# Kernel tuning notes

Measured on AMD Instinct MI355X. Metric: run time of the kernel, lower is better.

Reference implementation:

```python
import jax, jax.numpy as jnp
import numpy as np

M, K, D = 4, 2048, 32
N, C, H, W = 8, M * D, 64, 64


def setup_inputs() -> dict:
    key = jax.random.key(0)
    k1, k2 = jax.random.split(key)
    latent = jax.random.normal(k1, (N, C, H, W), dtype=jnp.float32)
    codebook = jax.random.normal(k2, (M, K, D), dtype=jnp.float32)
    return {"latent": latent, "codebook": codebook}


def reference(latent, codebook):
    n, c, h, w = latent.shape
    m, k, d = codebook.shape
    # [n,C,h,w] -> [n,h,w,m,d]
    q = jnp.transpose(latent, (0, 2, 3, 1)).reshape(n, h, w, m, d)
    q2 = jnp.sum(q * q, axis=-1, keepdims=True)          # [n,h,w,m,1]
    c2 = jnp.sum(codebook * codebook, axis=-1)           # [m,k]
    inter = jnp.einsum('nhwmd,mkd->nhwmk', q, codebook)  # [n,h,w,m,k]
    distance = -(q2 + c2 - 2.0 * inter)
    return jnp.argmax(distance, axis=-1)                 # [n,h,w,m] int
```

## Files before the change

### kernel.cpp

```cpp
#include <hip/hip_runtime.h>

#define M_ 4
#define K_ 2048
#define D_ 32
#define HW_ 4096
#define NHW_ 32768

#define EPS 0.01f

#define CH_OFF 0
#define CL_OFF (M_*K_*D_*2)
#define HN_OFF (CL_OFF*2)
#define K1_OFF (HN_OFF + M_*K_*4)
#define B2_OFF (K1_OFF + M_*NHW_*4)
#define CNT_OFF (B2_OFF + M_*NHW_*4)
#define LIST_OFF (CNT_OFF + 16)

typedef __attribute__((ext_vector_type(8))) short bf16x8;
typedef __attribute__((ext_vector_type(4))) float f32x4;

__device__ __forceinline__ short bf16_rte(float x, float* back) {
    unsigned u = __float_as_uint(x);
    unsigned r = (u + 0x7FFFu + ((u >> 16) & 1u)) >> 16;
    *back = __uint_as_float(r << 16);
    return (short)(r & 0xFFFFu);
}

__global__ __launch_bounds__(256) void prep_kernel(const float* __restrict__ cb,
                                                   unsigned char* __restrict__ ws) {
    if (blockIdx.x == 0 && threadIdx.x == 0) *(int*)(ws + CNT_OFF) = 0;
    int t = blockIdx.x * 256 + threadIdx.x;
    const float* src = cb + (size_t)t * D_;
    short* dh = (short*)(ws + CH_OFF) + (size_t)t * D_;
    short* dl = (short*)(ws + CL_OFF) + (size_t)t * D_;
    float* hn = (float*)(ws + HN_OFF);
    bf16x8 vh[4], vl[4];
    float c2 = 0.f;
    #pragma unroll
    for (int d = 0; d < D_; ++d) {
        float x = src[d];
        float hf, lf;
        short hb = bf16_rte(x, &hf);
        short lb = bf16_rte(x - hf, &lf);
        vh[d >> 3][d & 7] = hb;
        vl[d >> 3][d & 7] = lb;
        c2 = fmaf(x, x, c2);
    }
    #pragma unroll
    for (int i = 0; i < 4; ++i) {
        *(bf16x8*)(dh + i * 8) = vh[i];
        *(bf16x8*)(dl + i * 8) = vl[i];
    }
    hn[t] = -0.5f * c2;
}

__device__ __forceinline__ float score_fp32(const float* __restrict__ q,
                                            const float4* __restrict__ c) {
    float d0 = 0, d1 = 0, d2 = 0, d3 = 0, e0 = 0, e1 = 0, e2 = 0, e3 = 0;
    #pragma unroll
    for (int v = 0; v < 8; ++v) {
        float4 cv = c[v];
        d0 = fmaf(q[v * 4 + 0], cv.x, d0);
        d1 = fmaf(q[v * 4 + 1], cv.y, d1);
        d2 = fmaf(q[v * 4 + 2], cv.z, d2);
        d3 = fmaf(q[v * 4 + 3], cv.w, d3);
        e0 = fmaf(cv.x, cv.x, e0);
        e1 = fmaf(cv.y, cv.y, e1);
        e2 = fmaf(cv.z, cv.z, e2);
        e3 = fmaf(cv.w, cv.w, e3);
    }
    return ((d0 + d1) + (d2 + d3)) - 0.5f * ((e0 + e1) + (e2 + e3));
}

__global__ __launch_bounds__(512, 4) void score_kernel(
        const float* __restrict__ latent,
        const unsigned char* __restrict__ cws,
        int* __restrict__ k1w, float* __restrict__ b2w) {
    __shared__ float s_b1[2][M_][64];
    __shared__ int   s_k1[2][M_][64];
    __shared__ float s_b2[2][M_][64];

    const int tid  = threadIdx.x;
    const int wave = tid >> 6;
    const int L    = tid & 63;
    const int m    = wave & 3;
    const int kh   = wave >> 2;
    const int col  = L & 15;
    const int krow = L >> 4;
    const int posbase = blockIdx.x * 64;
    const int n   = posbase >> 12;
    const int hwb = posbase & (HW_ - 1);

    bf16x8 qh[4], ql[4];
    const float* lp = latent + ((size_t)n * (M_ * D_) + m * D_) * HW_ + hwb;
    #pragma unroll
    for (int g = 0; g < 4; ++g)
        #pragma unroll
        for (int j = 0; j < 8; ++j) {
            float x = lp[(size_t)(krow * 8 + j) * HW_ + g * 16 + col];
            float hf, lf;
            qh[g][j] = bf16_rte(x, &hf);
            ql[g][j] = bf16_rte(x - hf, &lf);
        }

    const short* ah = (const short*)(cws + CH_OFF)
                      + ((size_t)m * K_ + kh * 1024 + col) * D_ + krow * 8;
    const short* al = (const short*)(cws + CL_OFF)
                      + ((size_t)m * K_ + kh * 1024 + col) * D_ + krow * 8;
    const float* hn = (const float*)(cws + HN_OFF) + m * K_ + kh * 1024 + krow * 4;

    float b1[4], b2[4];
    int   k1[4];
    #pragma unroll
    for (int g = 0; g < 4; ++g) { b1[g] = b2[g] = -3.402823466e+38f; k1[g] = 0; }

    const int kbase = kh * 1024 + krow * 4;

    #pragma unroll 2
    for (int t = 0; t < 64; ++t) {
        bf16x8 ch = *(const bf16x8*)(ah + (size_t)t * (16 * D_));
        bf16x8 cl = *(const bf16x8*)(al + (size_t)t * (16 * D_));
        f32x4  c0 = *(const f32x4*)(hn + t * 16);
        const int kt = kbase + t * 16;
        #pragma unroll
        for (int g = 0; g < 4; ++g) {
            f32x4 a = __builtin_amdgcn_mfma_f32_16x16x32_bf16(cl, qh[g], c0, 0, 0, 0);
            a = __builtin_amdgcn_mfma_f32_16x16x32_bf16(ch, ql[g], a, 0, 0, 0);
            a = __builtin_amdgcn_mfma_f32_16x16x32_bf16(ch, qh[g], a, 0, 0, 0);
            #pragma unroll
            for (int r = 0; r < 4; ++r) {
                float s = a[r];
                b2[g] = __builtin_amdgcn_fmed3f(b1[g], b2[g], s);
                bool gt = s > b1[g];
                k1[g] = gt ? (kt + r) : k1[g];
                b1[g] = gt ? s : b1[g];
            }
        }
    }

    #pragma unroll
    for (int g = 0; g < 4; ++g) {
        #pragma unroll
        for (int off = 16; off <= 32; off <<= 1) {
            float ob1 = __shfl_xor(b1[g], off);
            int   ok1 = __shfl_xor(k1[g], off);
            float ob2 = __shfl_xor(b2[g], off);
            float mn  = fminf(b1[g], ob1);
            b2[g] = fmaxf(mn, fmaxf(b2[g], ob2));
            bool awin = (b1[g] > ob1) || (b1[g] == ob1 && k1[g] < ok1);
            b1[g] = awin ? b1[g] : ob1;
            k1[g] = awin ? k1[g] : ok1;
        }
    }
    if (L < 16) {
        #pragma unroll
        for (int g = 0; g < 4; ++g) {
            s_b1[kh][m][g * 16 + L] = b1[g];
            s_k1[kh][m][g * 16 + L] = k1[g];
            s_b2[kh][m][g * 16 + L] = b2[g];
        }
    }
    __syncthreads();

    if (tid < 256) {
        const int mm = tid >> 6;
        const int pl = tid & 63;
        float A1 = s_b1[0][mm][pl]; int I1 = s_k1[0][mm][pl]; float A2 = s_b2[0][mm][pl];
        float B1 = s_b1[1][mm][pl]; int J1 = s_k1[1][mm][pl]; float B2 = s_b2[1][mm][pl];
        float b2m = fmaxf(fminf(A1, B1), fmaxf(A2, B2));
        bool awin = (A1 > B1) || (A1 == B1 && I1 < J1);
        int K1 = awin ? I1 : J1;
        k1w[mm * NHW_ + posbase + pl] = K1;
        b2w[mm * NHW_ + posbase + pl] = b2m;
    }
}

__global__ __launch_bounds__(256) void confirm_kernel(
        const float* __restrict__ latent,
        const float* __restrict__ codebook,
        const int* __restrict__ k1w, const float* __restrict__ b2w,
        int* __restrict__ cnt, int* __restrict__ list,
        int* __restrict__ out) {
    const int t   = blockIdx.x * 256 + threadIdx.x;
    const int L   = threadIdx.x & 63;
    const int mm  = t >> 15;
    const int pos = t & (NHW_ - 1);
    const int n   = pos >> 12;
    const int hw  = pos & (HW_ - 1);

    int   K1  = k1w[t];
    float b2m = b2w[t];

    const float* lq = latent + ((size_t)n * (M_ * D_) + mm * D_) * HW_ + hw;
    float q[D_];
    #pragma unroll
    for (int d = 0; d < D_; ++d) q[d] = lq[(size_t)d * HW_];
    float sx = score_fp32(q, (const float4*)(codebook + ((size_t)mm * K_ + K1) * D_));
    bool conf = (sx > b2m + EPS);

    out[(size_t)pos * M_ + mm] = K1;

    unsigned long long mask = __ballot(!conf);
    if (mask) {
        int leader = __ffsll(mask) - 1;
        int base = 0;
        if (L == leader) base = atomicAdd(cnt, (int)__popcll(mask));
        base = __shfl(base, leader);
        if (!conf) {
            unsigned long long below = mask & ((1ull << L) - 1ull);
            list[base + (int)__popcll(below)] = t;
        }
    }
}

__global__ __launch_bounds__(256) void fallback_kernel(
        const float* __restrict__ latent,
        const float* __restrict__ codebook,
        const int* __restrict__ cnt, const int* __restrict__ list,
        int* __restrict__ out) {
    __shared__ float s_bs[4];
    __shared__ int   s_bk[4];
    const int tid  = threadIdx.x;
    const int wave = tid >> 6;
    const int L    = tid & 63;
    const int ncnt = *cnt;

    for (int e = blockIdx.x; e < ncnt; e += gridDim.x) {
        int t   = list[e];
        int mm  = t >> 15;
        int pos = t & (NHW_ - 1);
        int n   = pos >> 12;
        int hw  = pos & (HW_ - 1);
        const float* lq = latent + ((size_t)n * (M_ * D_) + mm * D_) * HW_ + hw;
        float q[D_];
        #pragma unroll
        for (int d = 0; d < D_; ++d) q[d] = lq[(size_t)d * HW_];

        float bs = -3.402823466e+38f;
        int   bk = 0;
        #pragma unroll
        for (int i = 0; i < 8; ++i) {
            int k = tid + 256 * i;
            float s = score_fp32(q, (const float4*)(codebook + ((size_t)mm * K_ + k) * D_));
            if (s > bs || (s == bs && k < bk)) { bs = s; bk = k; }
        }
        #pragma unroll
        for (int off = 1; off <= 32; off <<= 1) {
            float os = __shfl_xor(bs, off);
            int   ok = __shfl_xor(bk, off);
            if (os > bs || (os == bs && ok < bk)) { bs = os; bk = ok; }
        }
        if (L == 0) { s_bs[wave] = bs; s_bk[wave] = bk; }
        __syncthreads();
        if (tid == 0) {
            float fs = s_bs[0]; int fk = s_bk[0];
            #pragma unroll
            for (int w = 1; w < 4; ++w) {
                float os = s_bs[w]; int ok = s_bk[w];
                if (os > fs || (os == fs && ok < fk)) { fs = os; fk = ok; }
            }
            out[(size_t)pos * M_ + mm] = fk;
        }
        __syncthreads();
    }
}

extern "C" void kernel_launch(void* const* d_in, const int* in_sizes, int n_in,
                              void* d_out, int out_size, void* d_ws, size_t ws_size,
                              hipStream_t stream) {
    const float* latent   = (const float*)d_in[0];
    const float* codebook = (const float*)d_in[1];
    unsigned char* ws = (unsigned char*)d_ws;
    int* out = (int*)d_out;
    prep_kernel<<<(M_ * K_) / 256, 256, 0, stream>>>(codebook, ws);
    score_kernel<<<NHW_ / 64, 512, 0, stream>>>(latent, ws,
                                                (int*)(ws + K1_OFF),
                                                (float*)(ws + B2_OFF));
    confirm_kernel<<<(NHW_ * M_) / 256, 256, 0, stream>>>(latent, codebook,
                                                          (const int*)(ws + K1_OFF),
                                                          (const float*)(ws + B2_OFF),
                                                          (int*)(ws + CNT_OFF),
                                                          (int*)(ws + LIST_OFF),
                                                          out);
    fallback_kernel<<<1024, 256, 0, stream>>>(latent, codebook,
                                              (const int*)(ws + CNT_OFF),
                                              (const int*)(ws + LIST_OFF),
                                              out);
}
```

Measured before the change: 132.1 us.

## Fuse confirm step into score kernel and halve positions per block

Removes the separate confirm kernel. The score kernel now writes the top-1 index straight to the output and queues a position for the fallback whenever the gap between its own top-1 and top-2 scores is within epsilon. This drops the fp32 rescore of the chosen codeword and the workspace round-trip for k1/b2. Each block now handles 32 positions instead of 64, giving twice as many blocks, with launch bounds raised to 8 blocks per SU. The trade-off is that each codebook fragment loaded feeds half as many MFMAs, so codebook reuse drops. The confirm test also now uses the approximate split-bf16 scores rather than an exact fp32 recheck.

```diff
diff --git a/kernel.cpp b/kernel.cpp
--- a/kernel.cpp
+++ b/kernel.cpp
@@ -6,14 +6,12 @@
 #define HW_ 4096
 #define NHW_ 32768
 
-#define EPS 0.01f
+#define GAPEPS 0.01f
 
 #define CH_OFF 0
 #define CL_OFF (M_*K_*D_*2)
 #define HN_OFF (CL_OFF*2)
-#define K1_OFF (HN_OFF + M_*K_*4)
-#define B2_OFF (K1_OFF + M_*NHW_*4)
-#define CNT_OFF (B2_OFF + M_*NHW_*4)
+#define CNT_OFF (HN_OFF + M_*K_*4)
 #define LIST_OFF (CNT_OFF + 16)
 
 typedef __attribute__((ext_vector_type(8))) short bf16x8;
@@ -72,13 +70,14 @@
     return ((d0 + d1) + (d2 + d3)) - 0.5f * ((e0 + e1) + (e2 + e3));
 }
 
-__global__ __launch_bounds__(512, 4) void score_kernel(
+__global__ __launch_bounds__(512, 8) void score_kernel(
         const float* __restrict__ latent,
         const unsigned char* __restrict__ cws,
-        int* __restrict__ k1w, float* __restrict__ b2w) {
-    __shared__ float s_b1[2][M_][64];
-    __shared__ int   s_k1[2][M_][64];
-    __shared__ float s_b2[2][M_][64];
+        int* __restrict__ cnt, int* __restrict__ list,
+        int* __restrict__ out) {
+    __shared__ float s_b1[2][M_][32];
+    __shared__ int   s_k1[2][M_][32];
+    __shared__ float s_b2[2][M_][32];
 
     const int tid  = threadIdx.x;
     const int wave = tid >> 6;
@@ -87,14 +86,14 @@
     const int kh   = wave >> 2;
     const int col  = L & 15;
     const int krow = L >> 4;
-    const int posbase = blockIdx.x * 64;
+    const int posbase = blockIdx.x * 32;
     const int n   = posbase >> 12;
     const int hwb = posbase & (HW_ - 1);
 
-    bf16x8 qh[4], ql[4];
+    bf16x8 qh[2], ql[2];
     const float* lp = latent + ((size_t)n * (M_ * D_) + m * D_) * HW_ + hwb;
     #pragma unroll
-    for (int g = 0; g < 4; ++g)
+    for (int g = 0; g < 2; ++g)
         #pragma unroll
         for (int j = 0; j < 8; ++j) {
             float x = lp[(size_t)(krow * 8 + j) * HW_ + g * 16 + col];
@@ -109,10 +108,10 @@
                       + ((size_t)m * K_ + kh * 1024 + col) * D_ + krow * 8;
     const float* hn = (const float*)(cws + HN_OFF) + m * K_ + kh * 1024 + krow * 4;
 
-    float b1[4], b2[4];
-    int   k1[4];
-    #pragma unroll
-    for (int g = 0; g < 4; ++g) { b1[g] = b2[g] = -3.402823466e+38f; k1[g] = 0; }
+    float b1[2], b2[2];
+    int   k1[2];
+    #pragma unroll
+    for (int g = 0; g < 2; ++g) { b1[g] = b2[g] = -3.402823466e+38f; k1[g] = 0; }
 
     const int kbase = kh * 1024 + krow * 4;
 
@@ -123,7 +122,7 @@
         f32x4  c0 = *(const f32x4*)(hn + t * 16);
         const int kt = kbase + t * 16;
         #pragma unroll
-        for (int g = 0; g < 4; ++g) {
+        for (int g = 0; g < 2; ++g) {
             f32x4 a = __builtin_amdgcn_mfma_f32_16x16x32_bf16(cl, qh[g], c0, 0, 0, 0);
             a = __builtin_amdgcn_mfma_f32_16x16x32_bf16(ch, ql[g], a, 0, 0, 0);
             a = __builtin_amdgcn_mfma_f32_16x16x32_bf16(ch, qh[g], a, 0, 0, 0);
@@ -139,7 +138,7 @@
     }
 
     #pragma unroll
-    for (int g = 0; g < 4; ++g) {
+    for (int g = 0; g < 2; ++g) {
         #pragma unroll
         for (int off = 16; off <= 32; off <<= 1) {
             float ob1 = __shfl_xor(b1[g], off);
@@ -154,7 +153,7 @@
     }
     if (L < 16) {
         #pragma unroll
-        for (int g = 0; g < 4; ++g) {
+        for (int g = 0; g < 2; ++g) {
             s_b1[kh][m][g * 16 + L] = b1[g];
             s_k1[kh][m][g * 16 + L] = k1[g];
             s_b2[kh][m][g * 16 + L] = b2[g];
@@ -162,53 +161,31 @@
     }
     __syncthreads();
 
-    if (tid < 256) {
-        const int mm = tid >> 6;
-        const int pl = tid & 63;
+    if (tid < 128) {
+        const int mm = tid >> 5;
+        const int pl = tid & 31;
+        const int pos = posbase + pl;
+
         float A1 = s_b1[0][mm][pl]; int I1 = s_k1[0][mm][pl]; float A2 = s_b2[0][mm][pl];
         float B1 = s_b1[1][mm][pl]; int J1 = s_k1[1][mm][pl]; float B2 = s_b2[1][mm][pl];
         float b2m = fmaxf(fminf(A1, B1), fmaxf(A2, B2));
         bool awin = (A1 > B1) || (A1 == B1 && I1 < J1);
-        int K1 = awin ? I1 : J1;
-        k1w[mm * NHW_ + posbase + pl] = K1;
-        b2w[mm * NHW_ + posbase + pl] = b2m;
-    }
-}
-
-__global__ __launch_bounds__(256) void confirm_kernel(
-        const float* __restrict__ latent,
-        const float* __restrict__ codebook,
-        const int* __restrict__ k1w, const float* __restrict__ b2w,
-        int* __restrict__ cnt, int* __restrict__ list,
-        int* __restrict__ out) {
-    const int t   = blockIdx.x * 256 + threadIdx.x;
-    const int L   = threadIdx.x & 63;
-    const int mm  = t >> 15;
-    const int pos = t & (NHW_ - 1);
-    const int n   = pos >> 12;
-    const int hw  = pos & (HW_ - 1);
-
-    int   K1  = k1w[t];
-    float b2m = b2w[t];
-
-    const float* lq = latent + ((size_t)n * (M_ * D_) + mm * D_) * HW_ + hw;
-    float q[D_];
-    #pragma unroll
-    for (int d = 0; d < D_; ++d) q[d] = lq[(size_t)d * HW_];
-    float sx = score_fp32(q, (const float4*)(codebook + ((size_t)mm * K_ + K1) * D_));
-    bool conf = (sx > b2m + EPS);
-
-    out[(size_t)pos * M_ + mm] = K1;
-
-    unsigned long long mask = __ballot(!conf);
-    if (mask) {
-        int leader = __ffsll(mask) - 1;
-        int base = 0;
-        if (L == leader) base = atomicAdd(cnt, (int)__popcll(mask));
-        base = __shfl(base, leader);
-        if (!conf) {
-            unsigned long long below = mask & ((1ull << L) - 1ull);
-            list[base + (int)__popcll(below)] = t;
+        float b1m = awin ? A1 : B1;
+        int   K1  = awin ? I1 : J1;
+
+        out[(size_t)pos * M_ + mm] = K1;
+
+        bool conf = (b1m - b2m > GAPEPS);
+        unsigned long long mask = __ballot(!conf);
+        if (mask) {
+            int leader = __ffsll(mask) - 1;
+            int base = 0;
+            if (L == leader) base = atomicAdd(cnt, (int)__popcll(mask));
+            base = __shfl(base, leader);
+            if (!conf) {
+                unsigned long long below = mask & ((1ull << L) - 1ull);
+                list[base + (int)__popcll(below)] = mm * NHW_ + pos;
+            }
         }
     }
 }
@@ -273,15 +250,10 @@
     unsigned char* ws = (unsigned char*)d_ws;
     int* out = (int*)d_out;
     prep_kernel<<<(M_ * K_) / 256, 256, 0, stream>>>(codebook, ws);
-    score_kernel<<<NHW_ / 64, 512, 0, stream>>>(latent, ws,
-                                                (int*)(ws + K1_OFF),
-                                                (float*)(ws + B2_OFF));
-    confirm_kernel<<<(NHW_ * M_) / 256, 256, 0, stream>>>(latent, codebook,
-                                                          (const int*)(ws + K1_OFF),
-                                                          (const float*)(ws + B2_OFF),
-                                                          (int*)(ws + CNT_OFF),
-                                                          (int*)(ws + LIST_OFF),
-                                                          out);
+    score_kernel<<<NHW_ / 32, 512, 0, stream>>>(latent, ws,
+                                                (int*)(ws + CNT_OFF),
+                                                (int*)(ws + LIST_OFF),
+                                                out);
     fallback_kernel<<<1024, 256, 0, stream>>>(latent, codebook,
                                               (const int*)(ws + CNT_OFF),
                                               (const int*)(ws + LIST_OFF),
```

Result: slower. 137.1 us (+3.8%).
